# Optimization experiments

Hardware: AMD Instinct MI355X
Metric: run time of the kernel (lower is better)

## Reference

```python
import jax, jax.numpy as jnp
import numpy as np

B, S, D, H = 1, 4096, 768, 12
W_HEAD = D // H  # 64


def setup_inputs() -> dict:
    key = jax.random.key(0)
    k1, k2, k3 = jax.random.split(key, 3)
    x = jax.random.normal(k1, (B, S, D), dtype=jnp.float32)
    mask = jnp.ones((B, S), dtype=jnp.float32)
    W_qkv = jax.random.normal(k2, (D, 3 * D), dtype=jnp.float32) * (1.0 / np.sqrt(D))
    b_qkv = jax.random.normal(k3, (3 * D,), dtype=jnp.float32) * 0.02
    return {"x": x, "mask": mask, "W_qkv": W_qkv, "b_qkv": b_qkv}


def reference(x, mask, W_qkv, b_qkv):
    # fused QKV projection: (B,S,D) @ (D,3D) -> (B,S,3D)
    qkv = jnp.einsum('bsd,de->bse', x, W_qkv) + b_qkv
    q, k, v = jnp.split(qkv, 3, axis=-1)
    # split heads: (B,S,D) -> (B,H,S,W)
    def to_heads(t):
        return t.reshape(B, S, H, W_HEAD).transpose(0, 2, 1, 3)
    q, k, v = to_heads(q), to_heads(k), to_heads(v)
    scores = jnp.einsum('bhsw,bhtw->bhst', q, k) / np.sqrt(W_HEAD)
    # additive mask: mask (B,S) -> (B,1,1,S); 1 = keep
    scores = scores - 10000.0 * (1.0 - mask[:, None, None, :])
    scores = jax.nn.softmax(scores, axis=-1)
    h = jnp.einsum('bhst,bhtw->bhsw', scores, v)
    # merge heads: (B,H,S,W) -> (B,S,D)
    h = h.transpose(0, 2, 1, 3).reshape(B, S, D)
    return h
```

## Files before the change

kernel.cpp:

```cpp
#include <hip/hip_runtime.h>
#include <hip/hip_bf16.h>

namespace {
constexpr int S  = 4096;
constexpr int D  = 768;
constexpr int H  = 12;
constexpr int N3 = 2304;

typedef __bf16 bf16x4 __attribute__((ext_vector_type(4)));
typedef __bf16 bf16x8 __attribute__((ext_vector_type(8)));
typedef float  floatx4 __attribute__((ext_vector_type(4)));

__device__ inline void glds16(const __bf16* g, __bf16* l) {
  __builtin_amdgcn_global_load_lds(
      (const __attribute__((address_space(1))) void*)(const void*)g,
      (__attribute__((address_space(3))) void*)(void*)l, 16, 0, 0);
}

__global__ __launch_bounds__(256)
void convert_all(const float* __restrict__ x, __bf16* __restrict__ xb,
                 const float* __restrict__ W, __bf16* __restrict__ WT)
{
  const int bid = blockIdx.x;
  const int tid = threadIdx.x;
  if (bid < 3072) {
    const int i = (bid * 256 + tid) * 4;
    floatx4 v = *reinterpret_cast<const floatx4*>(x + i);
    bf16x4 b;
    #pragma unroll
    for (int e = 0; e < 4; ++e) b[e] = (__bf16)v[e];
    *reinterpret_cast<bf16x4*>(xb + i) = b;
  } else {
    __shared__ float T[64][65];
    const int b2 = bid - 3072;
    const int d0 = (b2 % 12) * 64, e0 = (b2 / 12) * 64;
    const int rr = tid >> 4, c4 = (tid & 15) * 4;
    #pragma unroll
    for (int it = 0; it < 4; ++it) {
      int d = it * 16 + rr;
      floatx4 v = *reinterpret_cast<const floatx4*>(W + (d0 + d) * N3 + e0 + c4);
      #pragma unroll
      for (int e = 0; e < 4; ++e) T[d][c4 + e] = v[e];
    }
    __syncthreads();
    #pragma unroll
    for (int it = 0; it < 4; ++it) {
      int e = it * 16 + rr;
      bf16x4 b;
      #pragma unroll
      for (int i = 0; i < 4; ++i) b[i] = (__bf16)T[c4 + i][e];
      *reinterpret_cast<bf16x4*>(WT + (e0 + e) * D + d0 + c4) = b;
    }
  }
}

__global__ __launch_bounds__(256)
void qkv_gemm(const __bf16* __restrict__ xb, const __bf16* __restrict__ WT,
              const float* __restrict__ bq, __bf16* __restrict__ Qb,
              __bf16* __restrict__ Kb, __bf16* __restrict__ vT)
{
  __shared__ __bf16 smem[14336];
  __bf16* As = smem;
  __bf16* Bs = smem + 8192;

  const int tid  = threadIdx.x;
  const int wave = tid >> 6, lane = tid & 63;
  const int quad = lane >> 4, l16 = lane & 15;
  const int m_base = (wave >> 1) * 64;
  const int n_base = (wave & 1) * 48;
  const int bm = blockIdx.x, bn = blockIdx.y;
  const int srow = lane >> 3, sg = lane & 7;

  floatx4 acc[4][3];
  #pragma unroll
  for (int i = 0; i < 4; ++i)
    #pragma unroll
    for (int j = 0; j < 3; ++j) acc[i][j] = (floatx4){0.f, 0.f, 0.f, 0.f};

  for (int ks = 0; ks < 12; ++ks) {
    const int k0 = ks * 64;
    __syncthreads();
    #pragma unroll
    for (int it = 0; it < 4; ++it) {
      int rbase = it * 32 + wave * 8;
      int row = rbase + srow;
      glds16(xb + (size_t)(bm * 128 + row) * D + k0 + (sg ^ (row & 7)) * 8,
             As + rbase * 64);
    }
    #pragma unroll
    for (int it = 0; it < 3; ++it) {
      int rbase = it * 32 + wave * 8;
      int row = rbase + srow;
      glds16(WT + (size_t)(bn * 96 + row) * D + k0 + (sg ^ (row & 7)) * 8,
             Bs + rbase * 64);
    }
    __syncthreads();

    bf16x8 af[4][2], bfr[3][2];
    #pragma unroll
    for (int mt = 0; mt < 4; ++mt)
      #pragma unroll
      for (int kt = 0; kt < 2; ++kt) {
        int m = m_base + mt * 16 + l16;
        af[mt][kt] = *reinterpret_cast<const bf16x8*>(
            &As[m * 64 + ((((kt << 2) | quad) ^ (l16 & 7)) << 3)]);
      }
    #pragma unroll
    for (int nt = 0; nt < 3; ++nt)
      #pragma unroll
      for (int kt = 0; kt < 2; ++kt) {
        int n = n_base + nt * 16 + l16;
        bfr[nt][kt] = *reinterpret_cast<const bf16x8*>(
            &Bs[n * 64 + ((((kt << 2) | quad) ^ (l16 & 7)) << 3)]);
      }
    #pragma unroll
    for (int kt = 0; kt < 2; ++kt)
      #pragma unroll
      for (int mt = 0; mt < 4; ++mt)
        #pragma unroll
        for (int nt = 0; nt < 3; ++nt)
          acc[mt][nt] = __builtin_amdgcn_mfma_f32_16x16x32_bf16(
              af[mt][kt], bfr[nt][kt], acc[mt][nt], 0, 0, 0);
  }

  if (bn < 16) {
    #pragma unroll
    for (int nt = 0; nt < 3; ++nt) {
      int col = bn * 96 + n_base + nt * 16 + l16;
      float bias = bq[col];
      #pragma unroll
      for (int mt = 0; mt < 4; ++mt) {
        int row = bm * 128 + m_base + mt * 16 + quad * 4;
        #pragma unroll
        for (int r = 0; r < 4; ++r) {
          __bf16 v = (__bf16)(acc[mt][nt][r] + bias);
          if (bn < 8) Qb[(row + r) * D + col] = v;
          else        Kb[(row + r) * D + (col - D)] = v;
        }
      }
    }
  } else {
    __syncthreads();
    __bf16* vts = smem;
    #pragma unroll
    for (int nt = 0; nt < 3; ++nt) {
      int wl = n_base + nt * 16 + l16;
      float bias = bq[bn * 96 + wl];
      int sw = (wl & 7) << 3;
      #pragma unroll
      for (int mt = 0; mt < 4; ++mt) {
        #pragma unroll
        for (int r = 0; r < 4; ++r) {
          int tl = m_base + mt * 16 + quad * 4 + r;
          int pos = (tl & ~31) | (quad << 3) | ((tl & 16) >> 2) | r;
          vts[wl * 128 + (pos ^ sw)] = (__bf16)(acc[mt][nt][r] + bias);
        }
      }
    }
    __syncthreads();
    const int w0g = bn * 96 - 2 * D;
    #pragma unroll
    for (int it = 0; it < 6; ++it) {
      int c = it * 256 + tid;
      int wl = c >> 4, t0 = (c & 15) * 8;
      bf16x8 v = *reinterpret_cast<const bf16x8*>(
          &vts[wl * 128 + (t0 ^ ((wl & 7) << 3))]);
      *reinterpret_cast<bf16x8*>(
          &vT[(size_t)(w0g + wl) * S + bm * 128 + t0]) = v;
    }
  }
}

__global__ __launch_bounds__(256)
void attention(const __bf16* __restrict__ Qb, const __bf16* __restrict__ Kb,
               const __bf16* __restrict__ vT, const float* __restrict__ mask,
               float* __restrict__ out)
{
  __shared__ char smem[16384 + 16384 + 256];
  __bf16* Ks = (__bf16*)smem;
  __bf16* Vt = (__bf16*)(smem + 16384);
  float*  Ll = (float*)(smem + 32768);
  float*  Lo = (float*)smem;

  const int tid  = threadIdx.x;
  const int wave = tid >> 6, lane = tid & 63;
  const int quad = lane >> 4, l16 = lane & 15;
  const int qh = wave >> 1;
  const int th = wave & 1;
  const int qb = blockIdx.x, h = blockIdx.y;
  const int q0 = qb * 64;
  const int qcol = h * 64;
  const int srow = lane >> 3, sg = lane & 7;
  const int vrow = lane >> 4, vs = lane & 15;

  bf16x8 qf[2][2];
  #pragma unroll
  for (int nt = 0; nt < 2; ++nt)
    #pragma unroll
    for (int kt = 0; kt < 2; ++kt)
      qf[nt][kt] = *reinterpret_cast<const bf16x8*>(
          Qb + (q0 + qh * 32 + nt * 16 + l16) * D + qcol + kt * 32 + quad * 8);

  floatx4 accO[4][2];
  #pragma unroll
  for (int wt = 0; wt < 4; ++wt)
    #pragma unroll
    for (int nt = 0; nt < 2; ++nt) accO[wt][nt] = (floatx4){0.f, 0.f, 0.f, 0.f};
  float l_lane[2] = {0.f, 0.f};

  for (int j = 0; j < 32; ++j) {
    __syncthreads();
    #pragma unroll
    for (int it = 0; it < 4; ++it) {
      int rbase = it * 32 + wave * 8;
      int t = rbase + srow;
      glds16(Kb + (size_t)(j * 128 + t) * D + qcol + (sg ^ (t & 7)) * 8,
             Ks + rbase * 64);
      int wbase = it * 16 + wave * 4;
      int w = wbase + vrow;
      glds16(vT + (size_t)(qcol + w) * S + j * 128 + (vs ^ (w & 7)) * 8,
             Vt + wbase * 128);
    }
    __syncthreads();

    bf16x4 ps[4][2];
    #pragma unroll
    for (int mt = 0; mt < 4; ++mt) {
      int trow = th * 64 + mt * 16 + l16;
      bf16x8 kf[2];
      #pragma unroll
      for (int kt = 0; kt < 2; ++kt)
        kf[kt] = *reinterpret_cast<const bf16x8*>(
            &Ks[trow * 64 + ((((kt << 2) | quad) ^ (l16 & 7)) << 3)]);
      floatx4 mv = *reinterpret_cast<const floatx4*>(
          mask + j * 128 + th * 64 + mt * 16 + quad * 4);
      #pragma unroll
      for (int nt = 0; nt < 2; ++nt) {
        floatx4 s = (floatx4){0.f, 0.f, 0.f, 0.f};
        #pragma unroll
        for (int kt = 0; kt < 2; ++kt)
          s = __builtin_amdgcn_mfma_f32_16x16x32_bf16(kf[kt], qf[nt][kt], s, 0, 0, 0);
        #pragma unroll
        for (int r = 0; r < 4; ++r) {
          float p = __expf(s[r] * 0.125f - 10000.f * (1.f - mv[r]));
          l_lane[nt] += p;
          ps[mt][nt][r] = (__bf16)p;
        }
      }
    }

    #pragma unroll
    for (int u = 0; u < 2; ++u) {
      bf16x8 pf[2];
      #pragma unroll
      for (int nt = 0; nt < 2; ++nt)
        #pragma unroll
        for (int r = 0; r < 4; ++r) {
          pf[nt][r]     = ps[2 * u][nt][r];
          pf[nt][4 + r] = ps[2 * u + 1][nt][r];
        }
      #pragma unroll
      for (int wt = 0; wt < 4; ++wt) {
        int w = wt * 16 + l16;
        bf16x8 vf = *reinterpret_cast<const bf16x8*>(
            &Vt[w * 128 + (((th * 8 + u * 4 + quad) ^ (w & 7)) << 3)]);
        #pragma unroll
        for (int nt = 0; nt < 2; ++nt)
          accO[wt][nt] = __builtin_amdgcn_mfma_f32_16x16x32_bf16(
              vf, pf[nt], accO[wt][nt], 0, 0, 0);
      }
    }
  }

  #pragma unroll
  for (int nt = 0; nt < 2; ++nt) {
    l_lane[nt] += __shfl_xor(l_lane[nt], 16, 64);
    l_lane[nt] += __shfl_xor(l_lane[nt], 32, 64);
  }
  __syncthreads();
  if (th == 1) {
    float* dst = Lo + qh * (64 * 33);
    #pragma unroll
    for (int wt = 0; wt < 4; ++wt)
      #pragma unroll
      for (int nt = 0; nt < 2; ++nt)
        #pragma unroll
        for (int r = 0; r < 4; ++r)
          dst[(wt * 16 + quad * 4 + r) * 33 + nt * 16 + l16] = accO[wt][nt][r];
    if (quad == 0) {
      #pragma unroll
      for (int nt = 0; nt < 2; ++nt)
        Ll[qh * 32 + nt * 16 + l16] = l_lane[nt];
    }
  }
  __syncthreads();
  if (th == 0) {
    const float* src = Lo + qh * (64 * 33);
    float l_tot[2];
    #pragma unroll
    for (int nt = 0; nt < 2; ++nt)
      l_tot[nt] = l_lane[nt] + Ll[qh * 32 + nt * 16 + l16];
    #pragma unroll
    for (int wt = 0; wt < 4; ++wt)
      #pragma unroll
      for (int nt = 0; nt < 2; ++nt) {
        floatx4 o;
        #pragma unroll
        for (int r = 0; r < 4; ++r)
          o[r] = (accO[wt][nt][r] +
                  src[(wt * 16 + quad * 4 + r) * 33 + nt * 16 + l16]) / l_tot[nt];
        int row = q0 + qh * 32 + nt * 16 + l16;
        int col = qcol + wt * 16 + quad * 4;
        *reinterpret_cast<floatx4*>(&out[row * D + col]) = o;
      }
  }
}

}

extern "C" void kernel_launch(void* const* d_in, const int* in_sizes, int n_in,
                              void* d_out, int out_size, void* d_ws, size_t ws_size,
                              hipStream_t stream) {
  const float *x = nullptr, *mask = nullptr, *Wq = nullptr, *bq = nullptr;
  for (int i = 0; i < n_in; ++i) {
    switch (in_sizes[i]) {
      case 3145728: x    = (const float*)d_in[i]; break;
      case 4096:    mask = (const float*)d_in[i]; break;
      case 1769472: Wq   = (const float*)d_in[i]; break;
      case 2304:    bq   = (const float*)d_in[i]; break;
      default: break;
    }
  }

  __bf16* xb = (__bf16*)d_out;
  __bf16* WT = xb + (size_t)S * D;
  __bf16* Qb = (__bf16*)d_ws;
  __bf16* Kb = Qb + (size_t)S * D;
  __bf16* vT = Kb + (size_t)S * D;

  convert_all<<<3072 + 432, 256, 0, stream>>>(x, xb, Wq, WT);
  qkv_gemm   <<<dim3(S / 128, N3 / 96), 256, 0, stream>>>(xb, WT, bq, Qb, Kb, vT);
  attention  <<<dim3(S / 64, H), 256, 0, stream>>>(Qb, Kb, vT, mask, (float*)d_out);
}
```

Baseline: 178.5 us.

## Double-buffer QKV GEMM LDS tiles and use exp2 with folded softmax constants

The QKV projection GEMM now uses a K-step of 32 with two LDS buffers, so the next tile's global-to-LDS loads are issued while the current tile's MFMAs run, and the loop needs one barrier per step instead of two. The swizzle is changed to fit the 32-wide rows. In the attention kernel, the mask term is precomputed once per row group, and exp is replaced by exp2 of a single FMA with log2(e) folded into the scale and the mask constant. This trades more loop iterations and smaller tiles per step for latency hiding, and relies on the new swizzle staying free of bank conflicts.

```diff
diff --git a/kernel.cpp b/kernel.cpp
--- a/kernel.cpp
+++ b/kernel.cpp
@@ -60,8 +60,6 @@
               __bf16* __restrict__ Kb, __bf16* __restrict__ vT)
 {
   __shared__ __bf16 smem[14336];
-  __bf16* As = smem;
-  __bf16* Bs = smem + 8192;
 
   const int tid  = threadIdx.x;
   const int wave = tid >> 6, lane = tid & 63;
@@ -69,7 +67,8 @@
   const int m_base = (wave >> 1) * 64;
   const int n_base = (wave & 1) * 48;
   const int bm = blockIdx.x, bn = blockIdx.y;
-  const int srow = lane >> 3, sg = lane & 7;
+  const int gslot = (lane & 3) ^ ((lane >> 3) & 3);
+  const int srow4 = lane >> 2;
 
   floatx4 acc[4][3];
   #pragma unroll
@@ -77,50 +76,54 @@
     #pragma unroll
     for (int j = 0; j < 3; ++j) acc[i][j] = (floatx4){0.f, 0.f, 0.f, 0.f};
 
-  for (int ks = 0; ks < 12; ++ks) {
-    const int k0 = ks * 64;
-    __syncthreads();
-    #pragma unroll
-    for (int it = 0; it < 4; ++it) {
-      int rbase = it * 32 + wave * 8;
-      int row = rbase + srow;
-      glds16(xb + (size_t)(bm * 128 + row) * D + k0 + (sg ^ (row & 7)) * 8,
-             As + rbase * 64);
-    }
-    #pragma unroll
-    for (int it = 0; it < 3; ++it) {
-      int rbase = it * 32 + wave * 8;
-      int row = rbase + srow;
-      glds16(WT + (size_t)(bn * 96 + row) * D + k0 + (sg ^ (row & 7)) * 8,
-             Bs + rbase * 64);
-    }
-    __syncthreads();
-
-    bf16x8 af[4][2], bfr[3][2];
+  auto stage = [&](int ks, int b) {
+    const int k0 = ks * 32;
+    __bf16* Ab = smem + b * 4096;
+    __bf16* Bb = smem + 8192 + b * 3072;
+    #pragma unroll
+    for (int it = 0; it < 2; ++it) {
+      int rbase = it * 64 + wave * 16;
+      glds16(xb + (size_t)(bm * 128 + rbase + srow4) * D + k0 + gslot * 8,
+             Ab + rbase * 32);
+    }
+    {
+      int rbase = wave * 16;
+      glds16(WT + (size_t)(bn * 96 + rbase + srow4) * D + k0 + gslot * 8,
+             Bb + rbase * 32);
+    }
+    if (wave < 2) {
+      int rbase = 64 + wave * 16;
+      glds16(WT + (size_t)(bn * 96 + rbase + srow4) * D + k0 + gslot * 8,
+             Bb + rbase * 32);
+    }
+  };
+
+  stage(0, 0);
+  for (int ks = 0; ks < 24; ++ks) {
+    const int cur = ks & 1;
+    __syncthreads();
+    if (ks < 23) stage(ks + 1, cur ^ 1);
+    const __bf16* Ac = smem + cur * 4096;
+    const __bf16* Bc = smem + 8192 + cur * 3072;
+    bf16x8 af[4], bfr[3];
+    #pragma unroll
+    for (int mt = 0; mt < 4; ++mt) {
+      int m = m_base + mt * 16 + l16;
+      af[mt] = *reinterpret_cast<const bf16x8*>(
+          &Ac[m * 32 + ((quad ^ ((m >> 1) & 3)) << 3)]);
+    }
+    #pragma unroll
+    for (int nt = 0; nt < 3; ++nt) {
+      int n = n_base + nt * 16 + l16;
+      bfr[nt] = *reinterpret_cast<const bf16x8*>(
+          &Bc[n * 32 + ((quad ^ ((n >> 1) & 3)) << 3)]);
+    }
     #pragma unroll
     for (int mt = 0; mt < 4; ++mt)
       #pragma unroll
-      for (int kt = 0; kt < 2; ++kt) {
-        int m = m_base + mt * 16 + l16;
-        af[mt][kt] = *reinterpret_cast<const bf16x8*>(
-            &As[m * 64 + ((((kt << 2) | quad) ^ (l16 & 7)) << 3)]);
-      }
-    #pragma unroll
-    for (int nt = 0; nt < 3; ++nt)
-      #pragma unroll
-      for (int kt = 0; kt < 2; ++kt) {
-        int n = n_base + nt * 16 + l16;
-        bfr[nt][kt] = *reinterpret_cast<const bf16x8*>(
-            &Bs[n * 64 + ((((kt << 2) | quad) ^ (l16 & 7)) << 3)]);
-      }
-    #pragma unroll
-    for (int kt = 0; kt < 2; ++kt)
-      #pragma unroll
-      for (int mt = 0; mt < 4; ++mt)
-        #pragma unroll
-        for (int nt = 0; nt < 3; ++nt)
-          acc[mt][nt] = __builtin_amdgcn_mfma_f32_16x16x32_bf16(
-              af[mt][kt], bfr[nt][kt], acc[mt][nt], 0, 0, 0);
+      for (int nt = 0; nt < 3; ++nt)
+        acc[mt][nt] = __builtin_amdgcn_mfma_f32_16x16x32_bf16(
+            af[mt], bfr[nt], acc[mt][nt], 0, 0, 0);
   }
 
   if (bn < 16) {
@@ -192,6 +195,8 @@
   const int qcol = h * 64;
   const int srow = lane >> 3, sg = lane & 7;
   const int vrow = lane >> 4, vs = lane & 15;
+  constexpr float CS = 0.18033688011112042f;
+  constexpr float CM = 14426.950408889634f;
 
   bf16x8 qf[2][2];
   #pragma unroll
@@ -234,6 +239,9 @@
             &Ks[trow * 64 + ((((kt << 2) | quad) ^ (l16 & 7)) << 3)]);
       floatx4 mv = *reinterpret_cast<const floatx4*>(
           mask + j * 128 + th * 64 + mt * 16 + quad * 4);
+      floatx4 mb;
+      #pragma unroll
+      for (int r = 0; r < 4; ++r) mb[r] = (mv[r] - 1.f) * CM;
       #pragma unroll
       for (int nt = 0; nt < 2; ++nt) {
         floatx4 s = (floatx4){0.f, 0.f, 0.f, 0.f};
@@ -242,7 +250,7 @@
           s = __builtin_amdgcn_mfma_f32_16x16x32_bf16(kf[kt], qf[nt][kt], s, 0, 0, 0);
         #pragma unroll
         for (int r = 0; r < 4; ++r) {
-          float p = __expf(s[r] * 0.125f - 10000.f * (1.f - mv[r]));
+          float p = exp2f(fmaf(s[r], CS, mb[r]));
           l_lane[nt] += p;
           ps[mt][nt][r] = (__bf16)p;
         }
```

Measured after the change: 209.1 us. 17.1% more time.
